# Kernel tuning notes

Hardware: AMD Instinct MI355X
Metric: run time of the kernel (lower is better)

## Reference

```python
import jax, jax.numpy as jnp
import numpy as np

B, N, E = 2, 20000, 640000
FREL_DIMS = [16, 128, 64, 32, 16, 16]   # rel_in_dim -> ... -> 16 (message dim)
FDYN_DIMS = [30, 128, 64, 32, 16, 6]    # (dyn_in_dim=14 + 16) -> ... -> delta_dim=6


def _mlp(x, params):
    # FourLayerMLP: Linear+ReLU x4, final Linear (no activation)
    for w, b in params[:-1]:
        x = jax.nn.relu(x @ w + b)
    w, b = params[-1]
    return x @ w + b


def setup_inputs() -> dict:
    key = jax.random.key(0)
    ks = jax.random.split(key, 16)
    inp = {
        "dyn": jax.random.normal(ks[0], (B, N, 14), jnp.float32),
        "rel": jax.random.normal(ks[1], (B, E, 16), jnp.float32),
        "send": jax.random.randint(ks[2], (E,), 0, N, dtype=jnp.int64),
        "recv": jax.random.randint(ks[3], (E,), 0, N, dtype=jnp.int64),
    }
    ki = 4
    for name, dims in (("frel", FREL_DIMS), ("fdyn", FDYN_DIMS)):
        for li in range(5):
            inp[f"{name}_w{li}"] = 0.05 * jax.random.normal(ks[ki], (dims[li], dims[li + 1]), jnp.float32)
            inp[f"{name}_b{li}"] = jnp.zeros((dims[li + 1],), jnp.float32)
            ki += 1
    return inp


def reference(dyn, rel, send, recv,
              frel_w0, frel_b0, frel_w1, frel_b1, frel_w2, frel_b2,
              frel_w3, frel_b3, frel_w4, frel_b4,
              fdyn_w0, fdyn_b0, fdyn_w1, fdyn_b1, fdyn_w2, fdyn_b2,
              fdyn_w3, fdyn_b3, fdyn_w4, fdyn_b4):
    frel = [(frel_w0, frel_b0), (frel_w1, frel_b1), (frel_w2, frel_b2),
            (frel_w3, frel_b3), (frel_w4, frel_b4)]
    fdyn = [(fdyn_w0, fdyn_b0), (fdyn_w1, fdyn_b1), (fdyn_w2, fdyn_b2),
            (fdyn_w3, fdyn_b3), (fdyn_w4, fdyn_b4)]
    b, n, _ = dyn.shape
    msg = _mlp(rel, frel)                                      # [B, E, 16]
    # index_add_ over node dim, recv shared across batch
    agg = jnp.zeros((b, n, 16), dyn.dtype).at[:, recv].add(msg)  # [B, N, 16]
    return _mlp(jnp.concatenate([dyn, agg], axis=-1), fdyn)    # [B, N, 6]
```

## Files before the change

### kernel.cpp

```cpp
#include <hip/hip_runtime.h>

#define BB 2
#define NN 20000
#define EE 640000

using short8 = __attribute__((ext_vector_type(8))) short;
using f32x4  = __attribute__((ext_vector_type(4))) float;
typedef unsigned int uint;

__device__ __forceinline__ uint bf16_rne(float f) {
    uint u = __float_as_uint(f);
    return (u + 0x7fffu + ((u >> 16) & 1u)) >> 16;
}
__device__ __forceinline__ float bf16_f(uint h) { return __uint_as_float(h << 16); }
__device__ __forceinline__ void split2(float x, float y, uint& hi, uint& lo) {
    uint hx = bf16_rne(x), hy = bf16_rne(y);
    uint lx = bf16_rne(x - bf16_f(hx)), ly = bf16_rne(y - bf16_f(hy));
    hi = hx | (hy << 16);
    lo = lx | (ly << 16);
}

template<int KT>
__device__ __forceinline__ void loadB(const char* H, const char* L, int rowb, int emask,
                                      int li, int q, short8* bh, short8* bl) {
    const int sw = (li & emask) << 4;
    const char* rh = H + li * rowb;
    const char* rl = L + li * rowb;
#pragma unroll
    for (int kt = 0; kt < KT; ++kt) {
        const int off = (kt * 64 + q * 16) ^ sw;
        bh[kt] = *(const short8*)(rh + off);
        bl[kt] = *(const short8*)(rl + off);
    }
}

#define MFMA16(a, b, c) __builtin_amdgcn_mfma_f32_16x16x32_bf16(a, b, c, 0, 0, 0)

template<int KT, int MT, bool BIAS4>
__device__ __forceinline__ void do_layer(const char* __restrict__ wf, const float* __restrict__ bias,
                                         const short8* bh, const short8* bl,
                                         int lane, f32x4* acc, int nReal) {
    const int q = lane >> 4;
#pragma unroll
    for (int mt = 0; mt < MT; ++mt) {
        if constexpr (BIAS4) {
            const float4 bv = *(const float4*)(bias + mt * 16 + q * 4);
            acc[mt][0] = bv.x; acc[mt][1] = bv.y; acc[mt][2] = bv.z; acc[mt][3] = bv.w;
        } else {
#pragma unroll
            for (int r = 0; r < 4; ++r) {
                const int ch = mt * 16 + q * 4 + r;
                acc[mt][r] = (ch < nReal) ? bias[ch] : 0.0f;
            }
        }
    }
#pragma unroll
    for (int kt = 0; kt < KT; ++kt) {
        short8 wh[MT], wl[MT];
#pragma unroll
        for (int mt = 0; mt < MT; ++mt) {
            const char* p = wf + (size_t)(mt * KT + kt) * 2048 + lane * 16;
            wh[mt] = *(const short8*)p;
            wl[mt] = *(const short8*)(p + 1024);
        }
#pragma unroll
        for (int mt = 0; mt < MT; ++mt) acc[mt] = MFMA16(wh[mt], bh[kt], acc[mt]);
#pragma unroll
        for (int mt = 0; mt < MT; ++mt) acc[mt] = MFMA16(wh[mt], bl[kt], acc[mt]);
#pragma unroll
        for (int mt = 0; mt < MT; ++mt) acc[mt] = MFMA16(wl[mt], bh[kt], acc[mt]);
#pragma unroll
        for (int mt = 0; mt < MT; ++mt) acc[mt] = MFMA16(wl[mt], bl[kt], acc[mt]);
    }
}

template<int MT>
__device__ __forceinline__ void store_acts(char* H, char* L, int rowb, int emask,
                                           int lane, const f32x4* acc) {
    const int li = lane & 15, q = lane >> 4;
    const int sw = (li & emask) << 4;
    char* rh = H + li * rowb;
    char* rl = L + li * rowb;
#pragma unroll
    for (int mt = 0; mt < MT; ++mt) {
        const float v0 = fmaxf(acc[mt][0], 0.f), v1 = fmaxf(acc[mt][1], 0.f);
        const float v2 = fmaxf(acc[mt][2], 0.f), v3 = fmaxf(acc[mt][3], 0.f);
        uint h01, l01, h23, l23;
        split2(v0, v1, h01, l01);
        split2(v2, v3, h23, l23);
        const int off = (mt * 32 + q * 8) ^ sw;
        *(uint*)(rh + off) = h01; *(uint*)(rh + off + 4) = h23;
        *(uint*)(rl + off) = l01; *(uint*)(rl + off + 4) = l23;
    }
}

#define DECL_LDS \
    __shared__ __align__(16) char XH0[16 * 64];  __shared__ __align__(16) char XL0[16 * 64];  \
    __shared__ __align__(16) char XH1[16 * 256]; __shared__ __align__(16) char XL1[16 * 256]; \
    __shared__ __align__(16) char XH2[16 * 128]; __shared__ __align__(16) char XL2[16 * 128];

template<int CSR>
__global__ __launch_bounds__(64, 3) void edge_mlp(
    const float* __restrict__ rel, const int* __restrict__ recv, const int* __restrict__ posOf,
    const char* __restrict__ wfrag,
    const float* __restrict__ b0, const float* __restrict__ b1, const float* __restrict__ b2,
    const float* __restrict__ b3, const float* __restrict__ b4,
    float* __restrict__ outp ) {
    DECL_LDS
    const int lane = threadIdx.x;
    const int li = lane & 15, q = lane >> 4;
    const int b = blockIdx.x / (EE / 16);
    const int eg0 = (blockIdx.x % (EE / 16)) * 16;

    {
        const int e = lane >> 2, c = lane & 3;
        const float4 v = *(const float4*)(rel + ((size_t)b * EE + eg0 + e) * 16 + c * 4);
        uint h01, l01, h23, l23;
        split2(v.x, v.y, h01, l01);
        split2(v.z, v.w, h23, l23);
        const int sw = (e & 3) << 4;
        char* rh = XH0 + e * 64; char* rl = XL0 + e * 64;
        const int o = (c * 8) ^ sw;
        *(uint*)(rh + o) = h01; *(uint*)(rh + o + 4) = h23;
        *(uint*)(rl + o) = l01; *(uint*)(rl + o + 4) = l23;
        const int oz = (32 + c * 8) ^ sw;
        *(uint*)(rh + oz) = 0; *(uint*)(rh + oz + 4) = 0;
        *(uint*)(rl + oz) = 0; *(uint*)(rl + oz + 4) = 0;
    }
    short8 bh[4], bl[4];
    f32x4 a8[8], a4[4], a2[2], a1[1];

    loadB<1>(XH0, XL0, 64, 3, li, q, bh, bl);
    do_layer<1, 8, true>(wfrag + 0, b0, bh, bl, lane, a8, 128);
    store_acts<8>(XH1, XL1, 256, 7, lane, a8);

    loadB<4>(XH1, XL1, 256, 7, li, q, bh, bl);
    do_layer<4, 4, true>(wfrag + 16384, b1, bh, bl, lane, a4, 64);
    store_acts<4>(XH2, XL2, 128, 7, lane, a4);

    loadB<2>(XH2, XL2, 128, 7, li, q, bh, bl);
    do_layer<2, 2, true>(wfrag + 49152, b2, bh, bl, lane, a2, 32);
    store_acts<2>(XH0, XL0, 64, 3, lane, a2);

    loadB<1>(XH0, XL0, 64, 3, li, q, bh, bl);
    do_layer<1, 1, true>(wfrag + 57344, b3, bh, bl, lane, a1, 16);
    store_acts<1>(XH2, XL2, 128, 7, lane, a1);
    {
        const int sw = (li & 7) << 4;
        const int oz = (32 + q * 8) ^ sw;
        *(uint*)(XH2 + li * 128 + oz) = 0; *(uint*)(XH2 + li * 128 + oz + 4) = 0;
        *(uint*)(XL2 + li * 128 + oz) = 0; *(uint*)(XL2 + li * 128 + oz + 4) = 0;
    }
    loadB<1>(XH2, XL2, 128, 7, li, q, bh, bl);
    do_layer<1, 1, true>(wfrag + 59392, b4, bh, bl, lane, a1, 16);

    if (CSR) {
        const int pos = posOf[eg0 + li];
        float4 v;
        v.x = a1[0][0]; v.y = a1[0][1]; v.z = a1[0][2]; v.w = a1[0][3];
        *(float4*)(outp + ((size_t)b * EE + pos) * 16 + q * 4) = v;
    } else {
        const int nd = recv[eg0 + li];
        float* dst = outp + ((size_t)b * NN + nd) * 16 + q * 4;
        atomicAdd(dst + 0, a1[0][0]); atomicAdd(dst + 1, a1[0][1]);
        atomicAdd(dst + 2, a1[0][2]); atomicAdd(dst + 3, a1[0][3]);
    }
}

__global__ __launch_bounds__(64, 3) void node_mlp(
    const float* __restrict__ dyn, const float* __restrict__ agg,
    const char* __restrict__ wfrag,
    const float* __restrict__ b0, const float* __restrict__ b1, const float* __restrict__ b2,
    const float* __restrict__ b3, const float* __restrict__ b4,
    float* __restrict__ out) {
    DECL_LDS
    const int lane = threadIdx.x;
    const int li = lane & 15, q = lane >> 4;
    const int b = blockIdx.x / (NN / 16);
    const int ng0 = (blockIdx.x % (NN / 16)) * 16;

    {
        const int n = lane >> 2, p = lane & 3;
        const size_t dbase = ((size_t)b * NN + ng0 + n) * 14;
        const size_t abase = ((size_t)b * NN + ng0 + n) * 16;
        float qa0, qa1, qa2, qa3, qb0, qb1, qb2, qb3;
        if (p < 3) {
            const float2 u = *(const float2*)(dyn + dbase + 4 * p);
            const float2 w = *(const float2*)(dyn + dbase + 4 * p + 2);
            qa0 = u.x; qa1 = u.y; qa2 = w.x; qa3 = w.y;
            const float2 g0 = *(const float2*)(agg + abase + 2 + 4 * p);
            const float2 g1 = *(const float2*)(agg + abase + 4 + 4 * p);
            qb0 = g0.x; qb1 = g0.y; qb2 = g1.x; qb3 = g1.y;
        } else {
            const float2 u = *(const float2*)(dyn + dbase + 12);
            const float2 g = *(const float2*)(agg + abase + 0);
            qa0 = u.x; qa1 = u.y; qa2 = g.x; qa3 = g.y;
            const float2 g2 = *(const float2*)(agg + abase + 14);
            qb0 = g2.x; qb1 = g2.y; qb2 = 0.f; qb3 = 0.f;
        }
        const int sw = (n & 3) << 4;
        char* rh = XH0 + n * 64; char* rl = XL0 + n * 64;
        uint h01, l01, h23, l23;
        split2(qa0, qa1, h01, l01);
        split2(qa2, qa3, h23, l23);
        const int o = (p * 8) ^ sw;
        *(uint*)(rh + o) = h01; *(uint*)(rh + o + 4) = h23;
        *(uint*)(rl + o) = l01; *(uint*)(rl + o + 4) = l23;
        split2(qb0, qb1, h01, l01);
        split2(qb2, qb3, h23, l23);
        const int o2 = (32 + p * 8) ^ sw;
        *(uint*)(rh + o2) = h01; *(uint*)(rh + o2 + 4) = h23;
        *(uint*)(rl + o2) = l01; *(uint*)(rl + o2 + 4) = l23;
    }
    short8 bh[4], bl[4];
    f32x4 a8[8], a4[4], a2[2], a1[1];

    loadB<1>(XH0, XL0, 64, 3, li, q, bh, bl);
    do_layer<1, 8, true>(wfrag + 61440, b0, bh, bl, lane, a8, 128);
    store_acts<8>(XH1, XL1, 256, 7, lane, a8);

    loadB<4>(XH1, XL1, 256, 7, li, q, bh, bl);
    do_layer<4, 4, true>(wfrag + 77824, b1, bh, bl, lane, a4, 64);
    store_acts<4>(XH2, XL2, 128, 7, lane, a4);

    loadB<2>(XH2, XL2, 128, 7, li, q, bh, bl);
    do_layer<2, 2, true>(wfrag + 110592, b2, bh, bl, lane, a2, 32);
    store_acts<2>(XH0, XL0, 64, 3, lane, a2);

    loadB<1>(XH0, XL0, 64, 3, li, q, bh, bl);
    do_layer<1, 1, true>(wfrag + 118784, b3, bh, bl, lane, a1, 16);
    store_acts<1>(XH2, XL2, 128, 7, lane, a1);
    {
        const int sw = (li & 7) << 4;
        const int oz = (32 + q * 8) ^ sw;
        *(uint*)(XH2 + li * 128 + oz) = 0; *(uint*)(XH2 + li * 128 + oz + 4) = 0;
        *(uint*)(XL2 + li * 128 + oz) = 0; *(uint*)(XL2 + li * 128 + oz + 4) = 0;
    }
    loadB<1>(XH2, XL2, 128, 7, li, q, bh, bl);
    do_layer<1, 1, false>(wfrag + 120832, b4, bh, bl, lane, a1, 6);

    const int gn = ng0 + li;
#pragma unroll
    for (int r = 0; r < 4; ++r) {
        const int ch = q * 4 + r;
        if (ch < 6) out[((size_t)b * NN + gn) * 6 + ch] = a1[0][r];
    }
}

__global__ __launch_bounds__(64) void wprep(
    const float* w0f, const float* w1f, const float* w2f, const float* w3f, const float* w4f,
    const float* w0d, const float* w1d, const float* w2d, const float* w3d, const float* w4d,
    char* __restrict__ wfrag) {
    const int bid = blockIdx.x;
    const int lane = threadIdx.x;
    const int net = bid / 30;
    const int r = bid % 30;
    int l, base;
    if (r < 8)       { l = 0; base = 0; }
    else if (r < 24) { l = 1; base = 8; }
    else if (r < 28) { l = 2; base = 24; }
    else if (r < 29) { l = 3; base = 28; }
    else             { l = 4; base = 29; }
    const int KTs[5] = {1, 4, 2, 1, 1};
    const int Krf[5] = {16, 128, 64, 32, 16};
    const int Krd[5] = {30, 128, 64, 32, 16};
    const int Ncf[5] = {128, 64, 32, 16, 16};
    const int Ncd[5] = {128, 64, 32, 16, 6};
    const float* Wf[5] = {w0f, w1f, w2f, w3f, w4f};
    const float* Wd[5] = {w0d, w1d, w2d, w3d, w4d};
    const int KT = KTs[l];
    const int idx = r - base;
    const int mt = idx / KT, kt = idx % KT;
    const int Kreal = net ? Krd[l] : Krf[l];
    const int Ncol  = net ? Ncd[l] : Ncf[l];
    const float* W  = net ? Wd[l] : Wf[l];
    const int ch = mt * 16 + (lane & 15);
    uint hi[4], lo[4];
#pragma unroll
    for (int t = 0; t < 4; ++t) {
        float x = 0.f, y = 0.f;
        const int k0 = kt * 32 + (lane >> 4) * 8 + 2 * t;
        if (k0 < Kreal && ch < Ncol) x = W[(size_t)k0 * Ncol + ch];
        if (k0 + 1 < Kreal && ch < Ncol) y = W[(size_t)(k0 + 1) * Ncol + ch];
        split2(x, y, hi[t], lo[t]);
    }
    uint4 H; H.x = hi[0]; H.y = hi[1]; H.z = hi[2]; H.w = hi[3];
    uint4 L; L.x = lo[0]; L.y = lo[1]; L.z = lo[2]; L.w = lo[3];
    *(uint4*)(wfrag + (size_t)bid * 2048 + lane * 16) = H;
    *(uint4*)(wfrag + (size_t)bid * 2048 + 1024 + lane * 16) = L;
}

__global__ void count_k(const int* __restrict__ recv, int* __restrict__ counts) {
    const int e = blockIdx.x * 256 + threadIdx.x;
    if (e < EE) atomicAdd(&counts[recv[e]], 1);
}

__global__ __launch_bounds__(1024) void scan_k(const int* __restrict__ counts,
                                               int* __restrict__ start, int* __restrict__ cursor) {
    __shared__ int part[1024];
    const int t = threadIdx.x;
    const int lo = t * 20, hi = lo + 20 < NN ? lo + 20 : NN;
    int s = 0;
    for (int i = lo; i < hi; ++i) s += counts[i];
    part[t] = s;
    __syncthreads();
    for (int d = 1; d < 1024; d <<= 1) {
        int v = 0;
        if (t >= d) v = part[t - d];
        __syncthreads();
        part[t] += v;
        __syncthreads();
    }
    int run = t ? part[t - 1] : 0;
    for (int i = lo; i < hi; ++i) { start[i] = run; cursor[i] = run; run += counts[i]; }
    if (t == 0) start[NN] = EE;
}

__global__ void fill_k(const int* __restrict__ recv, int* __restrict__ cursor,
                       int* __restrict__ posOf) {
    const int e = blockIdx.x * 256 + threadIdx.x;
    if (e < EE) posOf[e] = atomicAdd(&cursor[recv[e]], 1);
}

__global__ void gather_k(const float* __restrict__ msg, const int* __restrict__ start,
                         float* __restrict__ agg) {
    const int t = blockIdx.x * 256 + threadIdx.x;
    if (t >= BB * NN * 4) return;
    const int oq = t & 3;
    const int bn = t >> 2;
    const int n = bn % NN, b = bn / NN;
    const int s = start[n], e = start[n + 1];
    float4 S; S.x = 0.f; S.y = 0.f; S.z = 0.f; S.w = 0.f;
    for (int i = s; i < e; ++i) {
        const float4 v = *(const float4*)(msg + ((size_t)b * EE + i) * 16 + oq * 4);
        S.x += v.x; S.y += v.y; S.z += v.z; S.w += v.w;
    }
    *(float4*)(agg + (size_t)bn * 16 + oq * 4) = S;
}

extern "C" void kernel_launch(void* const* d_in, const int* in_sizes, int n_in,
                              void* d_out, int out_size, void* d_ws, size_t ws_size,
                              hipStream_t stream) {
    const float* dyn = (const float*)d_in[0];
    const float* rel = (const float*)d_in[1];
    const int* recv = (const int*)d_in[3];

    const float* fw[5]; const float* fb[5]; const float* dw[5]; const float* db[5];
    for (int i = 0; i < 5; ++i) {
        fw[i] = (const float*)d_in[4 + 2 * i];
        fb[i] = (const float*)d_in[5 + 2 * i];
        dw[i] = (const float*)d_in[14 + 2 * i];
        db[i] = (const float*)d_in[15 + 2 * i];
    }

    char* ws = (char*)d_ws;
    char* wfrag = ws;
    const size_t MSG_OFF = 131072;
    const size_t MSG_SZ = (size_t)BB * EE * 16 * 4;
    const size_t POS_OFF = MSG_OFF + MSG_SZ;
    const size_t CNT_OFF = POS_OFF + (size_t)EE * 4;
    const size_t CUR_OFF = CNT_OFF + (size_t)NN * 4;
    const size_t STA_OFF = CUR_OFF + (size_t)NN * 4;
    const size_t AGG_OFF_CSR = STA_OFF + 80128;
    const size_t NEED = AGG_OFF_CSR + (size_t)BB * NN * 16 * 4;
    const bool csr = ws_size >= NEED;

    wprep<<<60, 64, 0, stream>>>(fw[0], fw[1], fw[2], fw[3], fw[4],
                                 dw[0], dw[1], dw[2], dw[3], dw[4], wfrag);

    float* agg;
    if (csr) {
        float* msg = (float*)(ws + MSG_OFF);
        int* posOf = (int*)(ws + POS_OFF);
        int* counts = (int*)(ws + CNT_OFF);
        int* cursor = (int*)(ws + CUR_OFF);
        int* start = (int*)(ws + STA_OFF);
        agg = (float*)(ws + AGG_OFF_CSR);

        hipMemsetAsync(counts, 0, (size_t)NN * 4, stream);
        count_k<<<(EE + 255) / 256, 256, 0, stream>>>(recv, counts);
        scan_k<<<1, 1024, 0, stream>>>(counts, start, cursor);
        fill_k<<<(EE + 255) / 256, 256, 0, stream>>>(recv, cursor, posOf);
        edge_mlp<1><<<BB * (EE / 16), 64, 0, stream>>>(
            rel, recv, posOf, wfrag, fb[0], fb[1], fb[2], fb[3], fb[4], msg);
        gather_k<<<(BB * NN * 4 + 255) / 256, 256, 0, stream>>>(msg, start, agg);
    } else {
        agg = (float*)(ws + MSG_OFF);
        hipMemsetAsync(agg, 0, (size_t)BB * NN * 16 * 4, stream);
        edge_mlp<0><<<BB * (EE / 16), 64, 0, stream>>>(
            rel, recv, nullptr, wfrag, fb[0], fb[1], fb[2], fb[3], fb[4], agg);
    }

    node_mlp<<<BB * (NN / 16), 64, 0, stream>>>(
        dyn, agg, wfrag, db[0], db[1], db[2], db[3], db[4], (float*)d_out);
}
```

Baseline: 540.2 us.

## Make edge MLP persistent with register-resident weights and drop lo*lo MFMA term

The edge MLP kernel becomes persistent: 4096 blocks loop over edge tiles with a grid stride and prefetch the next tile's rel row and index. All 30 weight fragments (hi and lo) are loaded once into registers instead of being reloaded from global memory for every tile. Separately, the low-by-low bf16 split product is dropped in both layer routines, saving a quarter of the MFMAs at a small cost in accuracy. The weights take a large share of registers (launch bounds drop to one block), so occupancy falls and spills are possible.

Result: faster. 523.2 us (-3.1%).

```diff
diff --git a/kernel.cpp b/kernel.cpp
--- a/kernel.cpp
+++ b/kernel.cpp
@@ -36,6 +36,26 @@
 
 #define MFMA16(a, b, c) __builtin_amdgcn_mfma_f32_16x16x32_bf16(a, b, c, 0, 0, 0)
 
+template<int KT, int MT, int WOFF>
+__device__ __forceinline__ void layer_r(const short8 (&wh)[30], const short8 (&wl)[30],
+                                        const float* __restrict__ bias, int q,
+                                        const short8* bh, const short8* bl, f32x4* acc) {
+#pragma unroll
+    for (int mt = 0; mt < MT; ++mt) {
+        const float4 bv = *(const float4*)(bias + mt * 16 + q * 4);
+        acc[mt][0] = bv.x; acc[mt][1] = bv.y; acc[mt][2] = bv.z; acc[mt][3] = bv.w;
+    }
+#pragma unroll
+    for (int kt = 0; kt < KT; ++kt) {
+#pragma unroll
+        for (int mt = 0; mt < MT; ++mt) acc[mt] = MFMA16(wh[WOFF + mt * KT + kt], bh[kt], acc[mt]);
+#pragma unroll
+        for (int mt = 0; mt < MT; ++mt) acc[mt] = MFMA16(wh[WOFF + mt * KT + kt], bl[kt], acc[mt]);
+#pragma unroll
+        for (int mt = 0; mt < MT; ++mt) acc[mt] = MFMA16(wl[WOFF + mt * KT + kt], bh[kt], acc[mt]);
+    }
+}
+
 template<int KT, int MT, bool BIAS4>
 __device__ __forceinline__ void do_layer(const char* __restrict__ wf, const float* __restrict__ bias,
                                          const short8* bh, const short8* bl,
@@ -69,8 +89,6 @@
         for (int mt = 0; mt < MT; ++mt) acc[mt] = MFMA16(wh[mt], bl[kt], acc[mt]);
 #pragma unroll
         for (int mt = 0; mt < MT; ++mt) acc[mt] = MFMA16(wl[mt], bh[kt], acc[mt]);
-#pragma unroll
-        for (int mt = 0; mt < MT; ++mt) acc[mt] = MFMA16(wl[mt], bl[kt], acc[mt]);
     }
 }
 
@@ -100,7 +118,7 @@
     __shared__ __align__(16) char XH2[16 * 128]; __shared__ __align__(16) char XL2[16 * 128];
 
 template<int CSR>
-__global__ __launch_bounds__(64, 3) void edge_mlp(
+__global__ __launch_bounds__(64, 1) void edge_mlp_r(
     const float* __restrict__ rel, const int* __restrict__ recv, const int* __restrict__ posOf,
     const char* __restrict__ wfrag,
     const float* __restrict__ b0, const float* __restrict__ b1, const float* __restrict__ b2,
@@ -109,61 +127,87 @@
     DECL_LDS
     const int lane = threadIdx.x;
     const int li = lane & 15, q = lane >> 4;
-    const int b = blockIdx.x / (EE / 16);
-    const int eg0 = (blockIdx.x % (EE / 16)) * 16;
-
+    const int se = lane >> 2, sc = lane & 3;
+
+    short8 wh[30], wl[30];
+#pragma unroll
+    for (int f = 0; f < 30; ++f) {
+        const char* pp = wfrag + (size_t)f * 2048 + lane * 16;
+        wh[f] = *(const short8*)pp;
+        wl[f] = *(const short8*)(pp + 1024);
+    }
+
+    constexpr int NP = BB * (EE / 16);
+    const int stride = gridDim.x;
+
+    int p = blockIdx.x;
+    if (p >= NP) return;
+    float4 rv; int idx0;
     {
-        const int e = lane >> 2, c = lane & 3;
-        const float4 v = *(const float4*)(rel + ((size_t)b * EE + eg0 + e) * 16 + c * 4);
-        uint h01, l01, h23, l23;
-        split2(v.x, v.y, h01, l01);
-        split2(v.z, v.w, h23, l23);
-        const int sw = (e & 3) << 4;
-        char* rh = XH0 + e * 64; char* rl = XL0 + e * 64;
-        const int o = (c * 8) ^ sw;
-        *(uint*)(rh + o) = h01; *(uint*)(rh + o + 4) = h23;
-        *(uint*)(rl + o) = l01; *(uint*)(rl + o + 4) = l23;
-        const int oz = (32 + c * 8) ^ sw;
-        *(uint*)(rh + oz) = 0; *(uint*)(rh + oz + 4) = 0;
-        *(uint*)(rl + oz) = 0; *(uint*)(rl + oz + 4) = 0;
-    }
-    short8 bh[4], bl[4];
-    f32x4 a8[8], a4[4], a2[2], a1[1];
-
-    loadB<1>(XH0, XL0, 64, 3, li, q, bh, bl);
-    do_layer<1, 8, true>(wfrag + 0, b0, bh, bl, lane, a8, 128);
-    store_acts<8>(XH1, XL1, 256, 7, lane, a8);
-
-    loadB<4>(XH1, XL1, 256, 7, li, q, bh, bl);
-    do_layer<4, 4, true>(wfrag + 16384, b1, bh, bl, lane, a4, 64);
-    store_acts<4>(XH2, XL2, 128, 7, lane, a4);
-
-    loadB<2>(XH2, XL2, 128, 7, li, q, bh, bl);
-    do_layer<2, 2, true>(wfrag + 49152, b2, bh, bl, lane, a2, 32);
-    store_acts<2>(XH0, XL0, 64, 3, lane, a2);
-
-    loadB<1>(XH0, XL0, 64, 3, li, q, bh, bl);
-    do_layer<1, 1, true>(wfrag + 57344, b3, bh, bl, lane, a1, 16);
-    store_acts<1>(XH2, XL2, 128, 7, lane, a1);
-    {
-        const int sw = (li & 7) << 4;
-        const int oz = (32 + q * 8) ^ sw;
-        *(uint*)(XH2 + li * 128 + oz) = 0; *(uint*)(XH2 + li * 128 + oz + 4) = 0;
-        *(uint*)(XL2 + li * 128 + oz) = 0; *(uint*)(XL2 + li * 128 + oz + 4) = 0;
-    }
-    loadB<1>(XH2, XL2, 128, 7, li, q, bh, bl);
-    do_layer<1, 1, true>(wfrag + 59392, b4, bh, bl, lane, a1, 16);
-
-    if (CSR) {
-        const int pos = posOf[eg0 + li];
-        float4 v;
-        v.x = a1[0][0]; v.y = a1[0][1]; v.z = a1[0][2]; v.w = a1[0][3];
-        *(float4*)(outp + ((size_t)b * EE + pos) * 16 + q * 4) = v;
-    } else {
-        const int nd = recv[eg0 + li];
-        float* dst = outp + ((size_t)b * NN + nd) * 16 + q * 4;
-        atomicAdd(dst + 0, a1[0][0]); atomicAdd(dst + 1, a1[0][1]);
-        atomicAdd(dst + 2, a1[0][2]); atomicAdd(dst + 3, a1[0][3]);
+        const int b = p / (EE / 16), eg0 = (p % (EE / 16)) * 16;
+        rv = *(const float4*)(rel + ((size_t)b * EE + eg0 + se) * 16 + sc * 4);
+        idx0 = CSR ? posOf[eg0 + li] : recv[eg0 + li];
+    }
+    while (true) {
+        const int b = p / (EE / 16);
+        const int pn = p + stride;
+        float4 rn = {0.f, 0.f, 0.f, 0.f}; int idxn = 0;
+        if (pn < NP) {
+            const int bn = pn / (EE / 16), egn = (pn % (EE / 16)) * 16;
+            rn = *(const float4*)(rel + ((size_t)bn * EE + egn + se) * 16 + sc * 4);
+            idxn = CSR ? posOf[egn + li] : recv[egn + li];
+        }
+        {
+            uint h01, l01, h23, l23;
+            split2(rv.x, rv.y, h01, l01);
+            split2(rv.z, rv.w, h23, l23);
+            const int sw = (se & 3) << 4;
+            char* rh = XH0 + se * 64; char* rl = XL0 + se * 64;
+            const int o = (sc * 8) ^ sw;
+            *(uint*)(rh + o) = h01; *(uint*)(rh + o + 4) = h23;
+            *(uint*)(rl + o) = l01; *(uint*)(rl + o + 4) = l23;
+            const int oz = (32 + sc * 8) ^ sw;
+            *(uint*)(rh + oz) = 0; *(uint*)(rh + oz + 4) = 0;
+            *(uint*)(rl + oz) = 0; *(uint*)(rl + oz + 4) = 0;
+        }
+        short8 bh[4], bl[4];
+        f32x4 a8[8], a4[4], a2[2], a1[1];
+
+        loadB<1>(XH0, XL0, 64, 3, li, q, bh, bl);
+        layer_r<1, 8, 0 >(wh, wl, b0, q, bh, bl, a8);
+        store_acts<8>(XH1, XL1, 256, 7, lane, a8);
+
+        loadB<4>(XH1, XL1, 256, 7, li, q, bh, bl);
+        layer_r<4, 4, 8 >(wh, wl, b1, q, bh, bl, a4);
+        store_acts<4>(XH2, XL2, 128, 7, lane, a4);
+
+        loadB<2>(XH2, XL2, 128, 7, li, q, bh, bl);
+        layer_r<2, 2, 24>(wh, wl, b2, q, bh, bl, a2);
+        store_acts<2>(XH0, XL0, 64, 3, lane, a2);
+
+        loadB<1>(XH0, XL0, 64, 3, li, q, bh, bl);
+        layer_r<1, 1, 28>(wh, wl, b3, q, bh, bl, a1);
+        store_acts<1>(XH2, XL2, 128, 7, lane, a1);
+        {
+            const int sw = (li & 7) << 4;
+            const int oz = (32 + q * 8) ^ sw;
+            *(uint*)(XH2 + li * 128 + oz) = 0; *(uint*)(XH2 + li * 128 + oz + 4) = 0;
+            *(uint*)(XL2 + li * 128 + oz) = 0; *(uint*)(XL2 + li * 128 + oz + 4) = 0;
+        }
+        loadB<1>(XH2, XL2, 128, 7, li, q, bh, bl);
+        layer_r<1, 1, 29>(wh, wl, b4, q, bh, bl, a1);
+
+        if (CSR) {
+            float4 v;
+            v.x = a1[0][0]; v.y = a1[0][1]; v.z = a1[0][2]; v.w = a1[0][3];
+            *(float4*)(outp + ((size_t)b * EE + idx0) * 16 + q * 4) = v;
+        } else {
+            float* dst = outp + ((size_t)b * NN + idx0) * 16 + q * 4;
+            atomicAdd(dst + 0, a1[0][0]); atomicAdd(dst + 1, a1[0][1]);
+            atomicAdd(dst + 2, a1[0][2]); atomicAdd(dst + 3, a1[0][3]);
+        }
+        if (pn >= NP) break;
+        p = pn; rv = rn; idx0 = idxn;
     }
 }
 
@@ -381,13 +425,13 @@
         count_k<<<(EE + 255) / 256, 256, 0, stream>>>(recv, counts);
         scan_k<<<1, 1024, 0, stream>>>(counts, start, cursor);
         fill_k<<<(EE + 255) / 256, 256, 0, stream>>>(recv, cursor, posOf);
-        edge_mlp<1><<<BB * (EE / 16), 64, 0, stream>>>(
+        edge_mlp_r<1><<<4096, 64, 0, stream>>>(
             rel, recv, posOf, wfrag, fb[0], fb[1], fb[2], fb[3], fb[4], msg);
         gather_k<<<(BB * NN * 4 + 255) / 256, 256, 0, stream>>>(msg, start, agg);
     } else {
         agg = (float*)(ws + MSG_OFF);
         hipMemsetAsync(agg, 0, (size_t)BB * NN * 16 * 4, stream);
-        edge_mlp<0><<<BB * (EE / 16), 64, 0, stream>>>(
+        edge_mlp_r<0><<<4096, 64, 0, stream>>>(
             rel, recv, nullptr, wfrag, fb[0], fb[1], fb[2], fb[3], fb[4], agg);
     }
 
```

## Persistent MLP kernels with register-resident weights, bias in LDS, dropping lo*lo term

Applied to the files above, without the earlier changes.

The edge and node MLP kernels become persistent grid-stride kernels. Each wave loads all 30 weight fragments (hi and lo bf16) into registers once and caches the biases in LDS, instead of reloading them from global memory for every 16-row tile. The edge kernel handles two tiles per iteration, interleaves their layers, and prefetches the next pair's inputs. The lo*lo MFMA term of the split-bf16 product is dropped, cutting MFMA work by a quarter at a small precision cost; the heavy register use forces occupancy down to one wave per launch bound.

After: 471.2 us. -12.8%, faster.

```diff
diff --git a/kernel.cpp b/kernel.cpp
--- a/kernel.cpp
+++ b/kernel.cpp
@@ -1,4 +1,5 @@
 #include <hip/hip_runtime.h>
+#include <hip/hip_bf16.h>
 
 #define BB 2
 #define NN 20000
@@ -8,16 +9,14 @@
 using f32x4  = __attribute__((ext_vector_type(4))) float;
 typedef unsigned int uint;
 
-__device__ __forceinline__ uint bf16_rne(float f) {
-    uint u = __float_as_uint(f);
-    return (u + 0x7fffu + ((u >> 16) & 1u)) >> 16;
-}
-__device__ __forceinline__ float bf16_f(uint h) { return __uint_as_float(h << 16); }
+__device__ __forceinline__ uint b16u(float x) {
+    return (uint)__bfloat16_as_ushort(__float2bfloat16(x));
+}
 __device__ __forceinline__ void split2(float x, float y, uint& hi, uint& lo) {
-    uint hx = bf16_rne(x), hy = bf16_rne(y);
-    uint lx = bf16_rne(x - bf16_f(hx)), ly = bf16_rne(y - bf16_f(hy));
+    const uint hx = b16u(x), hy = b16u(y);
     hi = hx | (hy << 16);
-    lo = lx | (ly << 16);
+    const float fx = __uint_as_float(hx << 16), fy = __uint_as_float(hy << 16);
+    lo = b16u(x - fx) | (b16u(y - fy) << 16);
 }
 
 template<int KT>
@@ -36,41 +35,23 @@
 
 #define MFMA16(a, b, c) __builtin_amdgcn_mfma_f32_16x16x32_bf16(a, b, c, 0, 0, 0)
 
-template<int KT, int MT, bool BIAS4>
-__device__ __forceinline__ void do_layer(const char* __restrict__ wf, const float* __restrict__ bias,
-                                         const short8* bh, const short8* bl,
-                                         int lane, f32x4* acc, int nReal) {
-    const int q = lane >> 4;
+template<int KT, int MT, int WOFF>
+__device__ __forceinline__ void layer_r(const short8 (&wh)[30], const short8 (&wl)[30],
+                                        const float* bias, int q,
+                                        const short8* bh, const short8* bl, f32x4* acc) {
 #pragma unroll
     for (int mt = 0; mt < MT; ++mt) {
-        if constexpr (BIAS4) {
-            const float4 bv = *(const float4*)(bias + mt * 16 + q * 4);
-            acc[mt][0] = bv.x; acc[mt][1] = bv.y; acc[mt][2] = bv.z; acc[mt][3] = bv.w;
-        } else {
-#pragma unroll
-            for (int r = 0; r < 4; ++r) {
-                const int ch = mt * 16 + q * 4 + r;
-                acc[mt][r] = (ch < nReal) ? bias[ch] : 0.0f;
-            }
-        }
+        const float4 bv = *(const float4*)(bias + mt * 16 + q * 4);
+        acc[mt][0] = bv.x; acc[mt][1] = bv.y; acc[mt][2] = bv.z; acc[mt][3] = bv.w;
     }
 #pragma unroll
     for (int kt = 0; kt < KT; ++kt) {
-        short8 wh[MT], wl[MT];
-#pragma unroll
-        for (int mt = 0; mt < MT; ++mt) {
-            const char* p = wf + (size_t)(mt * KT + kt) * 2048 + lane * 16;
-            wh[mt] = *(const short8*)p;
-            wl[mt] = *(const short8*)(p + 1024);
-        }
-#pragma unroll
-        for (int mt = 0; mt < MT; ++mt) acc[mt] = MFMA16(wh[mt], bh[kt], acc[mt]);
-#pragma unroll
-        for (int mt = 0; mt < MT; ++mt) acc[mt] = MFMA16(wh[mt], bl[kt], acc[mt]);
-#pragma unroll
-        for (int mt = 0; mt < MT; ++mt) acc[mt] = MFMA16(wl[mt], bh[kt], acc[mt]);
-#pragma unroll
-        for (int mt = 0; mt < MT; ++mt) acc[mt] = MFMA16(wl[mt], bl[kt], acc[mt]);
+#pragma unroll
+        for (int mt = 0; mt < MT; ++mt) acc[mt] = MFMA16(wh[WOFF + mt * KT + kt], bh[kt], acc[mt]);
+#pragma unroll
+        for (int mt = 0; mt < MT; ++mt) acc[mt] = MFMA16(wh[WOFF + mt * KT + kt], bl[kt], acc[mt]);
+#pragma unroll
+        for (int mt = 0; mt < MT; ++mt) acc[mt] = MFMA16(wl[WOFF + mt * KT + kt], bh[kt], acc[mt]);
     }
 }
 
@@ -94,156 +75,246 @@
     }
 }
 
-#define DECL_LDS \
-    __shared__ __align__(16) char XH0[16 * 64];  __shared__ __align__(16) char XL0[16 * 64];  \
-    __shared__ __align__(16) char XH1[16 * 256]; __shared__ __align__(16) char XL1[16 * 256]; \
-    __shared__ __align__(16) char XH2[16 * 128]; __shared__ __align__(16) char XL2[16 * 128];
+__device__ __forceinline__ void stage16(char* H, char* L, int se, int sc, float4 v) {
+    uint h01, l01, h23, l23;
+    split2(v.x, v.y, h01, l01);
+    split2(v.z, v.w, h23, l23);
+    const int sw = (se & 7) << 4;
+    char* rh = H + se * 128; char* rl = L + se * 128;
+    const int o = (sc * 8) ^ sw;
+    *(uint*)(rh + o) = h01; *(uint*)(rh + o + 4) = h23;
+    *(uint*)(rl + o) = l01; *(uint*)(rl + o + 4) = l23;
+    const int oz = (32 + sc * 8) ^ sw;
+    *(uint*)(rh + oz) = 0; *(uint*)(rh + oz + 4) = 0;
+    *(uint*)(rl + oz) = 0; *(uint*)(rl + oz + 4) = 0;
+}
+
+__device__ __forceinline__ void padX2(char* H, char* L, int li, int q) {
+    const int sw = (li & 7) << 4;
+    const int oz = (32 + q * 8) ^ sw;
+    *(uint*)(H + li * 128 + oz) = 0; *(uint*)(H + li * 128 + oz + 4) = 0;
+    *(uint*)(L + li * 128 + oz) = 0; *(uint*)(L + li * 128 + oz + 4) = 0;
+}
 
 template<int CSR>
-__global__ __launch_bounds__(64, 3) void edge_mlp(
+__global__ __launch_bounds__(64, 1) void edge_mlp2(
     const float* __restrict__ rel, const int* __restrict__ recv, const int* __restrict__ posOf,
     const char* __restrict__ wfrag,
     const float* __restrict__ b0, const float* __restrict__ b1, const float* __restrict__ b2,
     const float* __restrict__ b3, const float* __restrict__ b4,
-    float* __restrict__ outp ) {
-    DECL_LDS
+    float* __restrict__ outp) {
+    __shared__ __align__(16) char XA0H[16 * 128], XA0L[16 * 128];
+    __shared__ __align__(16) char XA1H[16 * 256], XA1L[16 * 256];
+    __shared__ __align__(16) char XA2H[16 * 128], XA2L[16 * 128];
+    __shared__ __align__(16) char XB0H[16 * 128], XB0L[16 * 128];
+    __shared__ __align__(16) char XB1H[16 * 256], XB1L[16 * 256];
+    __shared__ __align__(16) char XB2H[16 * 128], XB2L[16 * 128];
+    __shared__ __align__(16) float BIAS[256];
+
     const int lane = threadIdx.x;
     const int li = lane & 15, q = lane >> 4;
-    const int b = blockIdx.x / (EE / 16);
-    const int eg0 = (blockIdx.x % (EE / 16)) * 16;
-
+    const int se = lane >> 2, sc = lane & 3;
+
+    if (lane < 32)      *(float4*)&BIAS[lane * 4] = *(const float4*)(b0 + lane * 4);
+    else if (lane < 48) *(float4*)&BIAS[128 + (lane - 32) * 4] = *(const float4*)(b1 + (lane - 32) * 4);
+    else if (lane < 56) *(float4*)&BIAS[192 + (lane - 48) * 4] = *(const float4*)(b2 + (lane - 48) * 4);
+    else if (lane < 60) *(float4*)&BIAS[224 + (lane - 56) * 4] = *(const float4*)(b3 + (lane - 56) * 4);
+    else                *(float4*)&BIAS[240 + (lane - 60) * 4] = *(const float4*)(b4 + (lane - 60) * 4);
+
+    short8 wh[30], wl[30];
+#pragma unroll
+    for (int f = 0; f < 30; ++f) {
+        const char* pp = wfrag + (size_t)f * 2048 + lane * 16;
+        wh[f] = *(const short8*)pp;
+        wl[f] = *(const short8*)(pp + 1024);
+    }
+
+    constexpr int PPB = EE / 16;
+    constexpr int NPAIR = BB * PPB / 2;
+    const int G = gridDim.x;
+
+    int pr = blockIdx.x;
+    if (pr >= NPAIR) return;
+
+    float4 rvA, rvB; int ixA, ixB;
     {
-        const int e = lane >> 2, c = lane & 3;
-        const float4 v = *(const float4*)(rel + ((size_t)b * EE + eg0 + e) * 16 + c * 4);
-        uint h01, l01, h23, l23;
-        split2(v.x, v.y, h01, l01);
-        split2(v.z, v.w, h23, l23);
-        const int sw = (e & 3) << 4;
-        char* rh = XH0 + e * 64; char* rl = XL0 + e * 64;
-        const int o = (c * 8) ^ sw;
-        *(uint*)(rh + o) = h01; *(uint*)(rh + o + 4) = h23;
-        *(uint*)(rl + o) = l01; *(uint*)(rl + o + 4) = l23;
-        const int oz = (32 + c * 8) ^ sw;
-        *(uint*)(rh + oz) = 0; *(uint*)(rh + oz + 4) = 0;
-        *(uint*)(rl + oz) = 0; *(uint*)(rl + oz + 4) = 0;
-    }
-    short8 bh[4], bl[4];
-    f32x4 a8[8], a4[4], a2[2], a1[1];
-
-    loadB<1>(XH0, XL0, 64, 3, li, q, bh, bl);
-    do_layer<1, 8, true>(wfrag + 0, b0, bh, bl, lane, a8, 128);
-    store_acts<8>(XH1, XL1, 256, 7, lane, a8);
-
-    loadB<4>(XH1, XL1, 256, 7, li, q, bh, bl);
-    do_layer<4, 4, true>(wfrag + 16384, b1, bh, bl, lane, a4, 64);
-    store_acts<4>(XH2, XL2, 128, 7, lane, a4);
-
-    loadB<2>(XH2, XL2, 128, 7, li, q, bh, bl);
-    do_layer<2, 2, true>(wfrag + 49152, b2, bh, bl, lane, a2, 32);
-    store_acts<2>(XH0, XL0, 64, 3, lane, a2);
-
-    loadB<1>(XH0, XL0, 64, 3, li, q, bh, bl);
-    do_layer<1, 1, true>(wfrag + 57344, b3, bh, bl, lane, a1, 16);
-    store_acts<1>(XH2, XL2, 128, 7, lane, a1);
-    {
-        const int sw = (li & 7) << 4;
-        const int oz = (32 + q * 8) ^ sw;
-        *(uint*)(XH2 + li * 128 + oz) = 0; *(uint*)(XH2 + li * 128 + oz + 4) = 0;
-        *(uint*)(XL2 + li * 128 + oz) = 0; *(uint*)(XL2 + li * 128 + oz + 4) = 0;
-    }
-    loadB<1>(XH2, XL2, 128, 7, li, q, bh, bl);
-    do_layer<1, 1, true>(wfrag + 59392, b4, bh, bl, lane, a1, 16);
-
-    if (CSR) {
-        const int pos = posOf[eg0 + li];
-        float4 v;
-        v.x = a1[0][0]; v.y = a1[0][1]; v.z = a1[0][2]; v.w = a1[0][3];
-        *(float4*)(outp + ((size_t)b * EE + pos) * 16 + q * 4) = v;
-    } else {
-        const int nd = recv[eg0 + li];
-        float* dst = outp + ((size_t)b * NN + nd) * 16 + q * 4;
-        atomicAdd(dst + 0, a1[0][0]); atomicAdd(dst + 1, a1[0][1]);
-        atomicAdd(dst + 2, a1[0][2]); atomicAdd(dst + 3, a1[0][3]);
-    }
-}
-
-__global__ __launch_bounds__(64, 3) void node_mlp(
+        const int pA = 2 * pr;
+        const int bb = pA / PPB, e0 = (pA % PPB) * 16;
+        rvA = *(const float4*)(rel + ((size_t)bb * EE + e0 + se) * 16 + sc * 4);
+        rvB = *(const float4*)(rel + ((size_t)bb * EE + e0 + 16 + se) * 16 + sc * 4);
+        ixA = CSR ? posOf[e0 + li] : recv[e0 + li];
+        ixB = CSR ? posOf[e0 + 16 + li] : recv[e0 + 16 + li];
+    }
+
+    while (true) {
+        const int pA = 2 * pr;
+        const int bA = pA / PPB;
+        const int prn = pr + G;
+        const bool more = prn < NPAIR;
+        float4 rnA = {0.f, 0.f, 0.f, 0.f}, rnB = {0.f, 0.f, 0.f, 0.f};
+        int jxA = 0, jxB = 0;
+        if (more) {
+            const int pN = 2 * prn;
+            const int bb = pN / PPB, e0 = (pN % PPB) * 16;
+            rnA = *(const float4*)(rel + ((size_t)bb * EE + e0 + se) * 16 + sc * 4);
+            rnB = *(const float4*)(rel + ((size_t)bb * EE + e0 + 16 + se) * 16 + sc * 4);
+            jxA = CSR ? posOf[e0 + li] : recv[e0 + li];
+            jxB = CSR ? posOf[e0 + 16 + li] : recv[e0 + 16 + li];
+        }
+
+        stage16(XA0H, XA0L, se, sc, rvA);
+        stage16(XB0H, XB0L, se, sc, rvB);
+
+        short8 bhA[4], blA[4], bhB[4], blB[4];
+        f32x4 aA[8], aB[8];
+
+        loadB<1>(XA0H, XA0L, 128, 7, li, q, bhA, blA);
+        loadB<1>(XB0H, XB0L, 128, 7, li, q, bhB, blB);
+        layer_r<1, 8, 0>(wh, wl, BIAS + 0, q, bhA, blA, aA);
+        store_acts<8>(XA1H, XA1L, 256, 7, lane, aA);
+        layer_r<1, 8, 0>(wh, wl, BIAS + 0, q, bhB, blB, aB);
+        store_acts<8>(XB1H, XB1L, 256, 7, lane, aB);
+        loadB<4>(XA1H, XA1L, 256, 7, li, q, bhA, blA);
+        loadB<4>(XB1H, XB1L, 256, 7, li, q, bhB, blB);
+        layer_r<4, 4, 8>(wh, wl, BIAS + 128, q, bhA, blA, aA);
+        store_acts<4>(XA2H, XA2L, 128, 7, lane, aA);
+        layer_r<4, 4, 8>(wh, wl, BIAS + 128, q, bhB, blB, aB);
+        store_acts<4>(XB2H, XB2L, 128, 7, lane, aB);
+        loadB<2>(XA2H, XA2L, 128, 7, li, q, bhA, blA);
+        loadB<2>(XB2H, XB2L, 128, 7, li, q, bhB, blB);
+        layer_r<2, 2, 24>(wh, wl, BIAS + 192, q, bhA, blA, aA);
+        store_acts<2>(XA0H, XA0L, 128, 7, lane, aA);
+        layer_r<2, 2, 24>(wh, wl, BIAS + 192, q, bhB, blB, aB);
+        store_acts<2>(XB0H, XB0L, 128, 7, lane, aB);
+        loadB<1>(XA0H, XA0L, 128, 7, li, q, bhA, blA);
+        loadB<1>(XB0H, XB0L, 128, 7, li, q, bhB, blB);
+        layer_r<1, 1, 28>(wh, wl, BIAS + 224, q, bhA, blA, aA);
+        store_acts<1>(XA2H, XA2L, 128, 7, lane, aA);
+        layer_r<1, 1, 28>(wh, wl, BIAS + 224, q, bhB, blB, aB);
+        store_acts<1>(XB2H, XB2L, 128, 7, lane, aB);
+        padX2(XA2H, XA2L, li, q);
+        padX2(XB2H, XB2L, li, q);
+        loadB<1>(XA2H, XA2L, 128, 7, li, q, bhA, blA);
+        loadB<1>(XB2H, XB2L, 128, 7, li, q, bhB, blB);
+        layer_r<1, 1, 29>(wh, wl, BIAS + 240, q, bhA, blA, aA);
+        layer_r<1, 1, 29>(wh, wl, BIAS + 240, q, bhB, blB, aB);
+
+        if (CSR) {
+            float4 vA, vB;
+            vA.x = aA[0][0]; vA.y = aA[0][1]; vA.z = aA[0][2]; vA.w = aA[0][3];
+            vB.x = aB[0][0]; vB.y = aB[0][1]; vB.z = aB[0][2]; vB.w = aB[0][3];
+            *(float4*)(outp + ((size_t)bA * EE + ixA) * 16 + q * 4) = vA;
+            *(float4*)(outp + ((size_t)bA * EE + ixB) * 16 + q * 4) = vB;
+        } else {
+            float* dA = outp + ((size_t)bA * NN + ixA) * 16 + q * 4;
+            atomicAdd(dA + 0, aA[0][0]); atomicAdd(dA + 1, aA[0][1]);
+            atomicAdd(dA + 2, aA[0][2]); atomicAdd(dA + 3, aA[0][3]);
+            float* dB = outp + ((size_t)bA * NN + ixB) * 16 + q * 4;
+            atomicAdd(dB + 0, aB[0][0]); atomicAdd(dB + 1, aB[0][1]);
+            atomicAdd(dB + 2, aB[0][2]); atomicAdd(dB + 3, aB[0][3]);
+        }
+        if (!more) break;
+        pr = prn; rvA = rnA; rvB = rnB; ixA = jxA; ixB = jxB;
+    }
+}
+
+__global__ __launch_bounds__(64, 1) void node_mlp_r(
     const float* __restrict__ dyn, const float* __restrict__ agg,
     const char* __restrict__ wfrag,
     const float* __restrict__ b0, const float* __restrict__ b1, const float* __restrict__ b2,
     const float* __restrict__ b3, const float* __restrict__ b4,
     float* __restrict__ out) {
-    DECL_LDS
+    __shared__ __align__(16) char XH0[16 * 128], XL0[16 * 128];
+    __shared__ __align__(16) char XH1[16 * 256], XL1[16 * 256];
+    __shared__ __align__(16) char XH2[16 * 128], XL2[16 * 128];
+    __shared__ __align__(16) float BIAS[256];
+
     const int lane = threadIdx.x;
     const int li = lane & 15, q = lane >> 4;
-    const int b = blockIdx.x / (NN / 16);
-    const int ng0 = (blockIdx.x % (NN / 16)) * 16;
-
-    {
-        const int n = lane >> 2, p = lane & 3;
-        const size_t dbase = ((size_t)b * NN + ng0 + n) * 14;
-        const size_t abase = ((size_t)b * NN + ng0 + n) * 16;
-        float qa0, qa1, qa2, qa3, qb0, qb1, qb2, qb3;
-        if (p < 3) {
-            const float2 u = *(const float2*)(dyn + dbase + 4 * p);
-            const float2 w = *(const float2*)(dyn + dbase + 4 * p + 2);
-            qa0 = u.x; qa1 = u.y; qa2 = w.x; qa3 = w.y;
-            const float2 g0 = *(const float2*)(agg + abase + 2 + 4 * p);
-            const float2 g1 = *(const float2*)(agg + abase + 4 + 4 * p);
-            qb0 = g0.x; qb1 = g0.y; qb2 = g1.x; qb3 = g1.y;
-        } else {
-            const float2 u = *(const float2*)(dyn + dbase + 12);
-            const float2 g = *(const float2*)(agg + abase + 0);
-            qa0 = u.x; qa1 = u.y; qa2 = g.x; qa3 = g.y;
-            const float2 g2 = *(const float2*)(agg + abase + 14);
-            qb0 = g2.x; qb1 = g2.y; qb2 = 0.f; qb3 = 0.f;
+
+    if (lane < 32)      *(float4*)&BIAS[lane * 4] = *(const float4*)(b0 + lane * 4);
+    else if (lane < 48) *(float4*)&BIAS[128 + (lane - 32) * 4] = *(const float4*)(b1 + (lane - 32) * 4);
+    else if (lane < 56) *(float4*)&BIAS[192 + (lane - 48) * 4] = *(const float4*)(b2 + (lane - 48) * 4);
+    else if (lane < 60) *(float4*)&BIAS[224 + (lane - 56) * 4] = *(const float4*)(b3 + (lane - 56) * 4);
+    else if (lane == 60) *(float4*)&BIAS[240] = *(const float4*)(b4);
+    else if (lane == 61) { BIAS[244] = b4[4]; BIAS[245] = b4[5]; BIAS[246] = 0.f; BIAS[247] = 0.f; }
+    else { BIAS[248 + (lane - 62) * 4] = 0.f; BIAS[249 + (lane - 62) * 4] = 0.f;
+           BIAS[250 + (lane - 62) * 4] = 0.f; BIAS[251 + (lane - 62) * 4] = 0.f; }
+
+    short8 wh[30], wl[30];
+#pragma unroll
+    for (int f = 0; f < 30; ++f) {
+        const char* pp = wfrag + 61440 + (size_t)f * 2048 + lane * 16;
+        wh[f] = *(const short8*)pp;
+        wl[f] = *(const short8*)(pp + 1024);
+    }
+
+    constexpr int NPN = BB * (NN / 16);
+    for (int p = blockIdx.x; p < NPN; p += gridDim.x) {
+        const int b = p / (NN / 16);
+        const int ng0 = (p % (NN / 16)) * 16;
+        {
+            const int n = lane >> 2, p4 = lane & 3;
+            const size_t dbase = ((size_t)b * NN + ng0 + n) * 14;
+            const size_t abase = ((size_t)b * NN + ng0 + n) * 16;
+            float qa0, qa1, qa2, qa3, qb0, qb1, qb2, qb3;
+            if (p4 < 3) {
+                const float2 u = *(const float2*)(dyn + dbase + 4 * p4);
+                const float2 w = *(const float2*)(dyn + dbase + 4 * p4 + 2);
+                qa0 = u.x; qa1 = u.y; qa2 = w.x; qa3 = w.y;
+                const float2 g0 = *(const float2*)(agg + abase + 2 + 4 * p4);
+                const float2 g1 = *(const float2*)(agg + abase + 4 + 4 * p4);
+                qb0 = g0.x; qb1 = g0.y; qb2 = g1.x; qb3 = g1.y;
+            } else {
+                const float2 u = *(const float2*)(dyn + dbase + 12);
+                const float2 g = *(const float2*)(agg + abase + 0);
+                qa0 = u.x; qa1 = u.y; qa2 = g.x; qa3 = g.y;
+                const float2 g2 = *(const float2*)(agg + abase + 14);
+                qb0 = g2.x; qb1 = g2.y; qb2 = 0.f; qb3 = 0.f;
+            }
+            const int sw = (n & 7) << 4;
+            char* rh = XH0 + n * 128; char* rl = XL0 + n * 128;
+            uint h01, l01, h23, l23;
+            split2(qa0, qa1, h01, l01);
+            split2(qa2, qa3, h23, l23);
+            const int o = (p4 * 8) ^ sw;
+            *(uint*)(rh + o) = h01; *(uint*)(rh + o + 4) = h23;
+            *(uint*)(rl + o) = l01; *(uint*)(rl + o + 4) = l23;
+            split2(qb0, qb1, h01, l01);
+            split2(qb2, qb3, h23, l23);
+            const int o2 = (32 + p4 * 8) ^ sw;
+            *(uint*)(rh + o2) = h01; *(uint*)(rh + o2 + 4) = h23;
+            *(uint*)(rl + o2) = l01; *(uint*)(rl + o2 + 4) = l23;
         }
-        const int sw = (n & 3) << 4;
-        char* rh = XH0 + n * 64; char* rl = XL0 + n * 64;
-        uint h01, l01, h23, l23;
-        split2(qa0, qa1, h01, l01);
-        split2(qa2, qa3, h23, l23);
-        const int o = (p * 8) ^ sw;
-        *(uint*)(rh + o) = h01; *(uint*)(rh + o + 4) = h23;
-        *(uint*)(rl + o) = l01; *(uint*)(rl + o + 4) = l23;
-        split2(qb0, qb1, h01, l01);
-        split2(qb2, qb3, h23, l23);
-        const int o2 = (32 + p * 8) ^ sw;
-        *(uint*)(rh + o2) = h01; *(uint*)(rh + o2 + 4) = h23;
-        *(uint*)(rl + o2) = l01; *(uint*)(rl + o2 + 4) = l23;
-    }
-    short8 bh[4], bl[4];
-    f32x4 a8[8], a4[4], a2[2], a1[1];
-
-    loadB<1>(XH0, XL0, 64, 3, li, q, bh, bl);
-    do_layer<1, 8, true>(wfrag + 61440, b0, bh, bl, lane, a8, 128);
-    store_acts<8>(XH1, XL1, 256, 7, lane, a8);
-
-    loadB<4>(XH1, XL1, 256, 7, li, q, bh, bl);
-    do_layer<4, 4, true>(wfrag + 77824, b1, bh, bl, lane, a4, 64);
-    store_acts<4>(XH2, XL2, 128, 7, lane, a4);
-
-    loadB<2>(XH2, XL2, 128, 7, li, q, bh, bl);
-    do_layer<2, 2, true>(wfrag + 110592, b2, bh, bl, lane, a2, 32);
-    store_acts<2>(XH0, XL0, 64, 3, lane, a2);
-
-    loadB<1>(XH0, XL0, 64, 3, li, q, bh, bl);
-    do_layer<1, 1, true>(wfrag + 118784, b3, bh, bl, lane, a1, 16);
-    store_acts<1>(XH2, XL2, 128, 7, lane, a1);
-    {
-        const int sw = (li & 7) << 4;
-        const int oz = (32 + q * 8) ^ sw;
-        *(uint*)(XH2 + li * 128 + oz) = 0; *(uint*)(XH2 + li * 128 + oz + 4) = 0;
-        *(uint*)(XL2 + li * 128 + oz) = 0; *(uint*)(XL2 + li * 128 + oz + 4) = 0;
-    }
-    loadB<1>(XH2, XL2, 128, 7, li, q, bh, bl);
-    do_layer<1, 1, false>(wfrag + 120832, b4, bh, bl, lane, a1, 6);
-
-    const int gn = ng0 + li;
-#pragma unroll
-    for (int r = 0; r < 4; ++r) {
-        const int ch = q * 4 + r;
-        if (ch < 6) out[((size_t)b * NN + gn) * 6 + ch] = a1[0][r];
+        short8 bh[4], bl[4];
+        f32x4 acc[8];
+
+        loadB<1>(XH0, XL0, 128, 7, li, q, bh, bl);
+        layer_r<1, 8, 0>(wh, wl, BIAS + 0, q, bh, bl, acc);
+        store_acts<8>(XH1, XL1, 256, 7, lane, acc);
+
+        loadB<4>(XH1, XL1, 256, 7, li, q, bh, bl);
+        layer_r<4, 4, 8>(wh, wl, BIAS + 128, q, bh, bl, acc);
+        store_acts<4>(XH2, XL2, 128, 7, lane, acc);
+
+        loadB<2>(XH2, XL2, 128, 7, li, q, bh, bl);
+        layer_r<2, 2, 24>(wh, wl, BIAS + 192, q, bh, bl, acc);
+        store_acts<2>(XH0, XL0, 128, 7, lane, acc);
+
+        loadB<1>(XH0, XL0, 128, 7, li, q, bh, bl);
+        layer_r<1, 1, 28>(wh, wl, BIAS + 224, q, bh, bl, acc);
+        store_acts<1>(XH2, XL2, 128, 7, lane, acc);
+        padX2(XH2, XL2, li, q);
+
+        loadB<1>(XH2, XL2, 128, 7, li, q, bh, bl);
+        layer_r<1, 1, 29>(wh, wl, BIAS + 240, q, bh, bl, acc);
+
+        const int gn = ng0 + li;
+#pragma unroll
+        for (int r = 0; r < 4; ++r) {
+            const int ch = q * 4 + r;
+            if (ch < 6) out[((size_t)b * NN + gn) * 6 + ch] = acc[0][r];
+        }
     }
 }
 
@@ -381,16 +452,16 @@
         count_k<<<(EE + 255) / 256, 256, 0, stream>>>(recv, counts);
         scan_k<<<1, 1024, 0, stream>>>(counts, start, cursor);
         fill_k<<<(EE + 255) / 256, 256, 0, stream>>>(recv, cursor, posOf);
-        edge_mlp<1><<<BB * (EE / 16), 64, 0, stream>>>(
+        edge_mlp2<1><<<2048, 64, 0, stream>>>(
             rel, recv, posOf, wfrag, fb[0], fb[1], fb[2], fb[3], fb[4], msg);
         gather_k<<<(BB * NN * 4 + 255) / 256, 256, 0, stream>>>(msg, start, agg);
     } else {
         agg = (float*)(ws + MSG_OFF);
         hipMemsetAsync(agg, 0, (size_t)BB * NN * 16 * 4, stream);
-        edge_mlp<0><<<BB * (EE / 16), 64, 0, stream>>>(
+        edge_mlp2<0><<<2048, 64, 0, stream>>>(
             rel, recv, nullptr, wfrag, fb[0], fb[1], fb[2], fb[3], fb[4], agg);
     }
 
-    node_mlp<<<BB * (NN / 16), 64, 0, stream>>>(
+    node_mlp_r<<<1024, 64, 0, stream>>>(
         dyn, agg, wfrag, db[0], db[1], db[2], db[3], db[4], (float*)d_out);
 }
```
